# Kernel optimization log

Hardware: AMD Instinct MI355X
Metric: run time of the kernel (lower is better)

## Reference

```python
import jax, jax.numpy as jnp
import numpy as np

N_NODES = 50000
N_EDGES = 600000
F_IN = 128
HID = 128
N_GRAPHS = 512
N_CLASSES = 2


def _sage_conv(x, src, dst, Wl, Wr, b, n_nodes):
    # PyG SAGEConv (aggr='mean'): out = lin_l(mean_{j in N(i)} x_j) + lin_r(x_i)
    msg_sum = jax.ops.segment_sum(x[src], dst, num_segments=n_nodes)  # [N, F]
    deg = jax.ops.segment_sum(jnp.ones((src.shape[0],), x.dtype), dst, num_segments=n_nodes)
    agg = msg_sum / jnp.maximum(deg, 1.0)[:, None]
    return agg @ Wl + b + x @ Wr


def setup_inputs() -> dict:
    key = jax.random.key(0)
    ks = jax.random.split(key, 16)
    x = jax.random.normal(ks[0], (N_NODES, F_IN), dtype=jnp.float32)
    edge_index = jax.random.randint(ks[1], (2, N_EDGES), 0, N_NODES, dtype=jnp.int64)
    batch = jnp.sort(jax.random.randint(ks[2], (N_NODES,), 0, N_GRAPHS, dtype=jnp.int64))
    inp = {"x": x, "edge_index": edge_index, "batch": batch, "num_graphs": N_GRAPHS}
    # SAGEConv params (glorot-ish scale)
    dims = [(F_IN, HID), (HID, HID), (HID, HID), (HID, HID)]
    for i, (din, dout) in enumerate(dims, start=1):
        s = 1.0 / np.sqrt(din)
        inp[f"Wl{i}"] = jax.random.normal(ks[2 + 3 * i], (din, dout), dtype=jnp.float32) * s
        inp[f"Wr{i}"] = jax.random.normal(ks[3 + 3 * i], (din, dout), dtype=jnp.float32) * s
        inp[f"b{i}"] = jnp.zeros((dout,), dtype=jnp.float32)
    inp["Wf1"] = jax.random.normal(ks[3], (HID, 128), dtype=jnp.float32) / np.sqrt(HID)
    inp["bf1"] = jnp.zeros((128,), dtype=jnp.float32)
    inp["Wf2"] = jax.random.normal(ks[4], (128, N_CLASSES), dtype=jnp.float32) / np.sqrt(128.0)
    inp["bf2"] = jnp.zeros((N_CLASSES,), dtype=jnp.float32)
    return inp


def reference(x, edge_index, batch, num_graphs,
              Wl1, Wr1, b1, Wl2, Wr2, b2, Wl3, Wr3, b3, Wl4, Wr4, b4,
              Wf1, bf1, Wf2, bf2):
    src, dst = edge_index[0], edge_index[1]
    n = x.shape[0]
    h = jax.nn.relu(_sage_conv(x, src, dst, Wl1, Wr1, b1, n))
    h = jax.nn.relu(_sage_conv(h, src, dst, Wl2, Wr2, b2, n))
    h = jax.nn.relu(_sage_conv(h, src, dst, Wl3, Wr3, b3, n))
    h = jax.nn.relu(_sage_conv(h, src, dst, Wl4, Wr4, b4, n))
    # global_mean_pool over graphs
    pooled_sum = jax.ops.segment_sum(h, batch, num_segments=num_graphs)
    counts = jax.ops.segment_sum(jnp.ones((n,), h.dtype), batch, num_segments=num_graphs)
    pooled = pooled_sum / jnp.maximum(counts, 1.0)[:, None]
    emb = pooled @ Wf1 + bf1
    # dropout p=0.5 is identity in eval mode
    out = emb @ Wf2 + bf2
    return out
```

## Files before the change

### kernel.cpp

```cpp
#include <hip/hip_runtime.h>

#define N_NODES   50000
#define N_EDGES   600000
#define F         128
#define N_GRAPHS  512
#define MROWS     32
#define ASTRIDE   264
#define NB_SCAN   196
#define ECAP      1536

typedef short  short8 __attribute__((ext_vector_type(8)));
typedef short  short4_t __attribute__((ext_vector_type(4)));
typedef float  f32x4  __attribute__((ext_vector_type(4)));

__device__ __forceinline__ void split_bf16(float v, short& hi, short& lo) {
    unsigned u  = __float_as_uint(v);
    unsigned hb = u & 0xFFFF0000u;
    hi = (short)(u >> 16);
    float rem = v - __uint_as_float(hb);
    lo = (short)(__float_as_uint(rem) >> 16);
}

__device__ __forceinline__ void split4(float x, float y, float z, float w,
                                       short4_t& hi, short4_t& lo) {
    short h, l;
    split_bf16(x, h, l); hi[0] = h; lo[0] = l;
    split_bf16(y, h, l); hi[1] = h; lo[1] = l;
    split_bf16(z, h, l); hi[2] = h; lo[2] = l;
    split_bf16(w, h, l); hi[3] = h; lo[3] = l;
}

__global__ void deg_int_kernel(const int* __restrict__ dst, int* __restrict__ deg) {
    int e = blockIdx.x * blockDim.x + threadIdx.x;
    if (e < N_EDGES) atomicAdd(&deg[dst[e]], 1);
}

__global__ __launch_bounds__(256) void bsum_kernel(const int* __restrict__ deg,
                                                   int* __restrict__ bsum) {
    int i = blockIdx.x * 256 + threadIdx.x;
    int v = (i < N_NODES) ? deg[i] : 0;
    #pragma unroll
    for (int off = 32; off > 0; off >>= 1) v += __shfl_down(v, off, 64);
    __shared__ int wsum[4];
    int lane = threadIdx.x & 63, w = threadIdx.x >> 6;
    if (lane == 0) wsum[w] = v;
    __syncthreads();
    if (threadIdx.x == 0) bsum[blockIdx.x] = wsum[0] + wsum[1] + wsum[2] + wsum[3];
}

__global__ __launch_bounds__(256) void p2_kernel(
    int* __restrict__ bsum,
    const float* __restrict__ Wl0, const float* __restrict__ Wr0,
    const float* __restrict__ Wl1, const float* __restrict__ Wr1,
    const float* __restrict__ Wl2, const float* __restrict__ Wr2,
    const float* __restrict__ Wl3, const float* __restrict__ Wr3,
    short* __restrict__ wtbase)
{
    if (blockIdx.x == 0) {
        __shared__ int s[256];
        int t = threadIdx.x;
        int v = (t < NB_SCAN) ? bsum[t] : 0;
        s[t] = v;
        __syncthreads();
        for (int off = 1; off < 256; off <<= 1) {
            int x = s[t];
            int add = (t >= off) ? s[t - off] : 0;
            __syncthreads();
            s[t] = x + add;
            __syncthreads();
        }
        bsum[t] = (t == 0) ? 0 : s[t - 1];
    } else {
        int gt = (blockIdx.x - 1) * 256 + threadIdx.x;
        int l  = gt >> 15;
        int t  = gt & 32767;
        const float* Wl; const float* Wr;
        switch (l) {
            case 0:  Wl = Wl0; Wr = Wr0; break;
            case 1:  Wl = Wl1; Wr = Wr1; break;
            case 2:  Wl = Wl2; Wr = Wr2; break;
            default: Wl = Wl3; Wr = Wr3; break;
        }
        int n = t >> 8, k = t & 255;
        float w = (k < F) ? Wl[k * F + n] : Wr[(k - F) * F + n];
        short h, lo;
        split_bf16(w, h, lo);
        short* hi_plane = wtbase + (size_t)l * 65536;
        hi_plane[t]         = h;
        hi_plane[32768 + t] = lo;
    }
}

__global__ __launch_bounds__(256) void scan_apply_kernel(
    const int* __restrict__ deg, const int* __restrict__ boff,
    int* __restrict__ row_start, int* __restrict__ cursor,
    float* __restrict__ inv_deg)
{
    __shared__ int s[256];
    int b = blockIdx.x, t = threadIdx.x;
    int i = b * 256 + t;
    int d = (i < N_NODES) ? deg[i] : 0;
    s[t] = d;
    __syncthreads();
    for (int off = 1; off < 256; off <<= 1) {
        int x = s[t];
        int add = (t >= off) ? s[t - off] : 0;
        __syncthreads();
        s[t] = x + add;
        __syncthreads();
    }
    int excl = s[t] - d + boff[b];
    if (i < N_NODES) {
        row_start[i] = excl;
        cursor[i]    = excl;
        inv_deg[i]   = 1.0f / fmaxf((float)d, 1.0f);
    }
    if (b == 0 && t == 0) row_start[N_NODES] = N_EDGES;
}

__global__ void fill_kernel(const int* __restrict__ src, const int* __restrict__ dst,
                            int* __restrict__ cursor, int* __restrict__ eidx) {
    int e = blockIdx.x * blockDim.x + threadIdx.x;
    if (e < N_EDGES) {
        int p = atomicAdd(&cursor[dst[e]], 1);
        eidx[p] = src[e];
    }
}

__global__ __launch_bounds__(512) void layer_kernel(
    const float* __restrict__ h_in, const int* __restrict__ row_start,
    const int* __restrict__ eidx, const float* __restrict__ inv_deg,
    const short* __restrict__ wt_hi, const short* __restrict__ wt_lo,
    const float* __restrict__ b, float* __restrict__ h_out)
{
    __shared__ short Ahi[MROWS][ASTRIDE];
    __shared__ short Alo[MROWS][ASTRIDE];
    __shared__ int   eshare[ECAP];

    const int t    = threadIdx.x;
    const int base = blockIdx.x * MROWS;

    const int blk_end = (base + MROWS < N_NODES) ? base + MROWS : N_NODES;
    const int s_blk0  = row_start[base];
    const int s_blk1  = row_start[blk_end];
    const int ecnt    = s_blk1 - s_blk0;
    const bool use_lds = (ecnt <= ECAP);
    if (use_lds) {
        for (int i = t; i < ecnt; i += 512) eshare[i] = eidx[s_blk0 + i];
    }
    __syncthreads();

    {
        const int c4   = t & 31;
        const int rr   = t >> 5;
        const int rowA = base + rr;
        const int rowB = rowA + 16;
        const bool vB  = (rowB < N_NODES);

        int a0 = row_start[rowA] - s_blk0, a1 = row_start[rowA + 1] - s_blk0;
        int b0 = 0, b1 = 0;
        if (vB) { b0 = row_start[rowB] - s_blk0; b1 = row_start[rowB + 1] - s_blk0; }
        const int na = a1 - a0, nb = b1 - b0;

        float scA = inv_deg[rowA];
        float scB = vB ? inv_deg[rowB] : 0.0f;

        float4 sA = ((const float4*)(h_in + (size_t)rowA * F))[c4];
        float4 sB = {0, 0, 0, 0};
        if (vB) sB = ((const float4*)(h_in + (size_t)rowB * F))[c4];

        f32x4 aA = {0, 0, 0, 0}, aB = {0, 0, 0, 0};
        const int mx = na > nb ? na : nb;
        for (int eo = 0; eo < mx; eo += 4) {
            int   idxA[4], idxB[4];
            float mA[4], mB[4];
            #pragma unroll
            for (int u = 0; u < 4; ++u) {
                bool okA = (eo + u) < na;
                bool okB = (eo + u) < nb;
                int offA = okA ? a0 + eo + u : 0;
                int offB = okB ? b0 + eo + u : 0;
                int ia = use_lds ? eshare[offA] : eidx[s_blk0 + offA];
                int ib = use_lds ? eshare[offB] : eidx[s_blk0 + offB];
                idxA[u] = okA ? ia : 0;
                idxB[u] = okB ? ib : 0;
                mA[u] = okA ? 1.0f : 0.0f;
                mB[u] = okB ? 1.0f : 0.0f;
            }
            #pragma unroll
            for (int u = 0; u < 4; ++u) {
                float4 va = ((const float4*)(h_in + (size_t)idxA[u] * F))[c4];
                float4 vb = ((const float4*)(h_in + (size_t)idxB[u] * F))[c4];
                aA[0] = fmaf(va.x, mA[u], aA[0]);
                aA[1] = fmaf(va.y, mA[u], aA[1]);
                aA[2] = fmaf(va.z, mA[u], aA[2]);
                aA[3] = fmaf(va.w, mA[u], aA[3]);
                aB[0] = fmaf(vb.x, mB[u], aB[0]);
                aB[1] = fmaf(vb.y, mB[u], aB[1]);
                aB[2] = fmaf(vb.z, mB[u], aB[2]);
                aB[3] = fmaf(vb.w, mB[u], aB[3]);
            }
        }

        short4_t h4, l4;
        split4(aA[0] * scA, aA[1] * scA, aA[2] * scA, aA[3] * scA, h4, l4);
        *(short4_t*)&Ahi[rr][c4 * 4] = h4;
        *(short4_t*)&Alo[rr][c4 * 4] = l4;
        split4(sA.x, sA.y, sA.z, sA.w, h4, l4);
        *(short4_t*)&Ahi[rr][F + c4 * 4] = h4;
        *(short4_t*)&Alo[rr][F + c4 * 4] = l4;

        split4(aB[0] * scB, aB[1] * scB, aB[2] * scB, aB[3] * scB, h4, l4);
        *(short4_t*)&Ahi[rr + 16][c4 * 4] = h4;
        *(short4_t*)&Alo[rr + 16][c4 * 4] = l4;
        split4(sB.x, sB.y, sB.z, sB.w, h4, l4);
        *(short4_t*)&Ahi[rr + 16][F + c4 * 4] = h4;
        *(short4_t*)&Alo[rr + 16][F + c4 * 4] = l4;
    }
    __syncthreads();

    const int w    = t >> 6;
    const int lane = t & 63;
    const int m    = lane & 15;
    const int quad = lane >> 4;
    const int n0   = w * 16 + m;

    f32x4 acc0 = {0,0,0,0};
    f32x4 acc1 = {0,0,0,0};

    #pragma unroll
    for (int ks = 0; ks < 8; ++ks) {
        const int ko = ks * 32 + quad * 8;
        short8 ah0 = *(const short8*)&Ahi[m][ko];
        short8 ah1 = *(const short8*)&Ahi[16 + m][ko];
        short8 al0 = *(const short8*)&Alo[m][ko];
        short8 al1 = *(const short8*)&Alo[16 + m][ko];
        short8 bh  = *(const short8*)&wt_hi[(size_t)n0 * 256 + ko];
        short8 bl  = *(const short8*)&wt_lo[(size_t)n0 * 256 + ko];

        acc0 = __builtin_amdgcn_mfma_f32_16x16x32_bf16(ah0, bh, acc0, 0, 0, 0);
        acc0 = __builtin_amdgcn_mfma_f32_16x16x32_bf16(ah0, bl, acc0, 0, 0, 0);
        acc0 = __builtin_amdgcn_mfma_f32_16x16x32_bf16(al0, bh, acc0, 0, 0, 0);

        acc1 = __builtin_amdgcn_mfma_f32_16x16x32_bf16(ah1, bh, acc1, 0, 0, 0);
        acc1 = __builtin_amdgcn_mfma_f32_16x16x32_bf16(ah1, bl, acc1, 0, 0, 0);
        acc1 = __builtin_amdgcn_mfma_f32_16x16x32_bf16(al1, bh, acc1, 0, 0, 0);
    }

    float bj = b[n0];
    #pragma unroll
    for (int reg = 0; reg < 4; ++reg) {
        int r0 = base + quad * 4 + reg;
        int r1 = r0 + 16;
        if (r0 < N_NODES) h_out[(size_t)r0 * F + n0] = fmaxf(acc0[reg] + bj, 0.0f);
        if (r1 < N_NODES) h_out[(size_t)r1 * F + n0] = fmaxf(acc1[reg] + bj, 0.0f);
    }
}

__global__ __launch_bounds__(128) void poolhead_kernel(
    const int* __restrict__ batch, const float* __restrict__ h,
    const float* __restrict__ Wf1, const float* __restrict__ bf1,
    const float* __restrict__ Wf2, const float* __restrict__ bf2,
    float* __restrict__ out)
{
    int g = blockIdx.x;
    int j = threadIdx.x;
    int lo = 0, hi = N_NODES;
    while (lo < hi) { int m = (lo + hi) >> 1; if (batch[m] < g) lo = m + 1; else hi = m; }
    int start = lo;
    hi = N_NODES;
    while (lo < hi) { int m = (lo + hi) >> 1; if (batch[m] <= g) lo = m + 1; else hi = m; }
    int end = lo;

    float acc = 0.0f;
    int r = start;
    for (; r + 4 <= end; r += 4) {
        float v0 = h[(size_t)(r + 0) * F + j];
        float v1 = h[(size_t)(r + 1) * F + j];
        float v2 = h[(size_t)(r + 2) * F + j];
        float v3 = h[(size_t)(r + 3) * F + j];
        acc += (v0 + v1) + (v2 + v3);
    }
    for (; r < end; ++r) acc += h[(size_t)r * F + j];

    __shared__ float p[F];
    __shared__ float emb[F];
    p[j] = acc / fmaxf((float)(end - start), 1.0f);
    __syncthreads();
    float e = bf1[j];
    #pragma unroll 8
    for (int k = 0; k < F; ++k) e += p[k] * Wf1[k * F + j];
    emb[j] = e;
    __syncthreads();
    if (j < 2) {
        float o = bf2[j];
        for (int k = 0; k < F; ++k) o += emb[k] * Wf2[k * 2 + j];
        out[(size_t)g * 2 + j] = o;
    }
}

extern "C" void kernel_launch(void* const* d_in, const int* in_sizes, int n_in,
                              void* d_out, int out_size, void* d_ws, size_t ws_size,
                              hipStream_t stream) {
    const float* x     = (const float*)d_in[0];
    const int*   ei    = (const int*)d_in[1];
    const int*   src   = ei;
    const int*   dst   = ei + N_EDGES;
    const int*   batch = (const int*)d_in[2];
    const float* Wl[4] = {(const float*)d_in[4],  (const float*)d_in[7],
                          (const float*)d_in[10], (const float*)d_in[13]};
    const float* Wr[4] = {(const float*)d_in[5],  (const float*)d_in[8],
                          (const float*)d_in[11], (const float*)d_in[14]};
    const float* bb[4] = {(const float*)d_in[6],  (const float*)d_in[9],
                          (const float*)d_in[12], (const float*)d_in[15]};
    const float* Wf1 = (const float*)d_in[16];
    const float* bf1 = (const float*)d_in[17];
    const float* Wf2 = (const float*)d_in[18];
    const float* bf2 = (const float*)d_in[19];
    float* out = (float*)d_out;

    float* ws = (float*)d_ws;
    const size_t HSZ = (size_t)N_NODES * F;
    float* B0        = ws;
    float* B1        = B0 + HSZ;
    float* inv_deg   = B1 + HSZ;
    int*   row_start = (int*)(inv_deg + N_NODES);
    int*   cursor    = row_start + N_NODES + 1;
    int*   eidx      = cursor + N_NODES;
    int*   deg_i     = eidx + N_EDGES;
    int*   bsum      = deg_i + N_NODES;
    short* wtbase    = (short*)(bsum + 256);

    (void)hipMemsetAsync(deg_i, 0, N_NODES * sizeof(int), stream);

    deg_int_kernel<<<(N_EDGES + 255) / 256, 256, 0, stream>>>(dst, deg_i);
    bsum_kernel<<<NB_SCAN, 256, 0, stream>>>(deg_i, bsum);
    p2_kernel<<<513, 256, 0, stream>>>(bsum,
        Wl[0], Wr[0], Wl[1], Wr[1], Wl[2], Wr[2], Wl[3], Wr[3], wtbase);
    scan_apply_kernel<<<NB_SCAN, 256, 0, stream>>>(deg_i, bsum, row_start, cursor, inv_deg);
    fill_kernel<<<(N_EDGES + 255) / 256, 256, 0, stream>>>(src, dst, cursor, eidx);

    const int layer_blocks = (N_NODES + MROWS - 1) / MROWS;
    const float* hin = x;
    float* buf[2] = {B0, B1};
    for (int l = 0; l < 4; ++l) {
        float* tgt = buf[l & 1];
        const short* whi = wtbase + (size_t)l * 65536;
        const short* wlo = whi + 32768;
        layer_kernel<<<layer_blocks, 512, 0, stream>>>(
            hin, row_start, eidx, inv_deg, whi, wlo, bb[l], tgt);
        hin = tgt;
    }

    poolhead_kernel<<<N_GRAPHS, 128, 0, stream>>>(batch, hin, Wf1, bf1, Wf2, bf2, out);
}
```

Before: 469.8 us.

## Store node features in bf16 to halve gather traffic across layers

Converts the input features to bf16 in a new pre-pass, and stores every layer's output activations as bf16 instead of fp32. The neighbour gather and the pooling read packed bf16 and widen to fp32 for accumulation, so each gathered row moves half the bytes. The self term is no longer split into hi/lo parts, since it is already exact bf16. The gather is also restructured to one row per 16 threads with 8-wide edge unrolling, and the LDS staging of edge indices is dropped. The cost is lower precision in the activations and the risk of exceeding the accuracy tolerance.

```diff
diff --git a/kernel.cpp b/kernel.cpp
--- a/kernel.cpp
+++ b/kernel.cpp
@@ -7,11 +7,11 @@
 #define MROWS     32
 #define ASTRIDE   264
 #define NB_SCAN   196
-#define ECAP      1536
-
-typedef short  short8 __attribute__((ext_vector_type(8)));
-typedef short  short4_t __attribute__((ext_vector_type(4)));
-typedef float  f32x4  __attribute__((ext_vector_type(4)));
+
+typedef short          short8   __attribute__((ext_vector_type(8)));
+typedef short          short4_t __attribute__((ext_vector_type(4)));
+typedef float          f32x4    __attribute__((ext_vector_type(4)));
+typedef unsigned int   uint4_t  __attribute__((ext_vector_type(4)));
 
 __device__ __forceinline__ void split_bf16(float v, short& hi, short& lo) {
     unsigned u  = __float_as_uint(v);
@@ -21,18 +21,29 @@
     lo = (short)(__float_as_uint(rem) >> 16);
 }
 
-__device__ __forceinline__ void split4(float x, float y, float z, float w,
-                                       short4_t& hi, short4_t& lo) {
-    short h, l;
-    split_bf16(x, h, l); hi[0] = h; lo[0] = l;
-    split_bf16(y, h, l); hi[1] = h; lo[1] = l;
-    split_bf16(z, h, l); hi[2] = h; lo[2] = l;
-    split_bf16(w, h, l); hi[3] = h; lo[3] = l;
+__device__ __forceinline__ unsigned short f2bf_rne(float f) {
+    unsigned u = __float_as_uint(f);
+    u += 0x7FFFu + ((u >> 16) & 1u);
+    return (unsigned short)(u >> 16);
 }
 
 __global__ void deg_int_kernel(const int* __restrict__ dst, int* __restrict__ deg) {
     int e = blockIdx.x * blockDim.x + threadIdx.x;
     if (e < N_EDGES) atomicAdd(&deg[dst[e]], 1);
+}
+
+__global__ __launch_bounds__(256) void x2bf_kernel(const float* __restrict__ x,
+                                                   unsigned short* __restrict__ xb) {
+    int i = blockIdx.x * 256 + threadIdx.x;
+    if (i >= (N_NODES * F) / 8) return;
+    float4 a = ((const float4*)x)[2 * i];
+    float4 b = ((const float4*)x)[2 * i + 1];
+    short8 o;
+    o[0] = (short)f2bf_rne(a.x); o[1] = (short)f2bf_rne(a.y);
+    o[2] = (short)f2bf_rne(a.z); o[3] = (short)f2bf_rne(a.w);
+    o[4] = (short)f2bf_rne(b.x); o[5] = (short)f2bf_rne(b.y);
+    o[6] = (short)f2bf_rne(b.z); o[7] = (short)f2bf_rne(b.w);
+    ((short8*)xb)[i] = o;
 }
 
 __global__ __launch_bounds__(256) void bsum_kernel(const int* __restrict__ deg,
@@ -128,94 +139,74 @@
 }
 
 __global__ __launch_bounds__(512) void layer_kernel(
-    const float* __restrict__ h_in, const int* __restrict__ row_start,
+    const unsigned short* __restrict__ hb_in, const int* __restrict__ row_start,
     const int* __restrict__ eidx, const float* __restrict__ inv_deg,
     const short* __restrict__ wt_hi, const short* __restrict__ wt_lo,
-    const float* __restrict__ b, float* __restrict__ h_out)
+    const float* __restrict__ b, unsigned short* __restrict__ hb_out)
 {
     __shared__ short Ahi[MROWS][ASTRIDE];
     __shared__ short Alo[MROWS][ASTRIDE];
-    __shared__ int   eshare[ECAP];
 
     const int t    = threadIdx.x;
     const int base = blockIdx.x * MROWS;
 
-    const int blk_end = (base + MROWS < N_NODES) ? base + MROWS : N_NODES;
-    const int s_blk0  = row_start[base];
-    const int s_blk1  = row_start[blk_end];
-    const int ecnt    = s_blk1 - s_blk0;
-    const bool use_lds = (ecnt <= ECAP);
-    if (use_lds) {
-        for (int i = t; i < ecnt; i += 512) eshare[i] = eidx[s_blk0 + i];
-    }
-    __syncthreads();
-
     {
-        const int c4   = t & 31;
-        const int rr   = t >> 5;
-        const int rowA = base + rr;
-        const int rowB = rowA + 16;
-        const bool vB  = (rowB < N_NODES);
-
-        int a0 = row_start[rowA] - s_blk0, a1 = row_start[rowA + 1] - s_blk0;
-        int b0 = 0, b1 = 0;
-        if (vB) { b0 = row_start[rowB] - s_blk0; b1 = row_start[rowB + 1] - s_blk0; }
-        const int na = a1 - a0, nb = b1 - b0;
-
-        float scA = inv_deg[rowA];
-        float scB = vB ? inv_deg[rowB] : 0.0f;
-
-        float4 sA = ((const float4*)(h_in + (size_t)rowA * F))[c4];
-        float4 sB = {0, 0, 0, 0};
-        if (vB) sB = ((const float4*)(h_in + (size_t)rowB * F))[c4];
-
-        f32x4 aA = {0, 0, 0, 0}, aB = {0, 0, 0, 0};
-        const int mx = na > nb ? na : nb;
-        for (int eo = 0; eo < mx; eo += 4) {
-            int   idxA[4], idxB[4];
-            float mA[4], mB[4];
+        const int c8  = t & 15;
+        const int rr  = t >> 4;
+        const int row = base + rr;
+        const bool v  = (row < N_NODES);
+
+        int a0 = 0, na = 0;
+        float sc = 0.0f;
+        if (v) {
+            a0 = row_start[row];
+            na = row_start[row + 1] - a0;
+            sc = inv_deg[row];
+        }
+
+        short8 selfv = {0,0,0,0,0,0,0,0};
+        if (v) selfv = *(const short8*)(hb_in + (size_t)row * F + c8 * 8);
+
+        float acc[8] = {0,0,0,0,0,0,0,0};
+        for (int eo = 0; eo < na; eo += 8) {
+            int   idx[8];
+            float msk[8];
             #pragma unroll
-            for (int u = 0; u < 4; ++u) {
-                bool okA = (eo + u) < na;
-                bool okB = (eo + u) < nb;
-                int offA = okA ? a0 + eo + u : 0;
-                int offB = okB ? b0 + eo + u : 0;
-                int ia = use_lds ? eshare[offA] : eidx[s_blk0 + offA];
-                int ib = use_lds ? eshare[offB] : eidx[s_blk0 + offB];
-                idxA[u] = okA ? ia : 0;
-                idxB[u] = okB ? ib : 0;
-                mA[u] = okA ? 1.0f : 0.0f;
-                mB[u] = okB ? 1.0f : 0.0f;
+            for (int u = 0; u < 8; ++u) {
+                bool ok = (eo + u) < na;
+                int  sl = ok ? a0 + eo + u : a0;
+                int  ia = eidx[sl];
+                idx[u] = ok ? ia : 0;
+                msk[u] = ok ? 1.0f : 0.0f;
             }
             #pragma unroll
-            for (int u = 0; u < 4; ++u) {
-                float4 va = ((const float4*)(h_in + (size_t)idxA[u] * F))[c4];
-                float4 vb = ((const float4*)(h_in + (size_t)idxB[u] * F))[c4];
-                aA[0] = fmaf(va.x, mA[u], aA[0]);
-                aA[1] = fmaf(va.y, mA[u], aA[1]);
-                aA[2] = fmaf(va.z, mA[u], aA[2]);
-                aA[3] = fmaf(va.w, mA[u], aA[3]);
-                aB[0] = fmaf(vb.x, mB[u], aB[0]);
-                aB[1] = fmaf(vb.y, mB[u], aB[1]);
-                aB[2] = fmaf(vb.z, mB[u], aB[2]);
-                aB[3] = fmaf(vb.w, mB[u], aB[3]);
+            for (int u = 0; u < 8; ++u) {
+                short8 hv = *(const short8*)(hb_in + (size_t)idx[u] * F + c8 * 8);
+                uint4_t uw = *(const uint4_t*)&hv;
+                #pragma unroll
+                for (int q = 0; q < 4; ++q) {
+                    unsigned wq = uw[q];
+                    float flo = __uint_as_float(wq << 16);
+                    float fhi = __uint_as_float(wq & 0xFFFF0000u);
+                    acc[2 * q]     = fmaf(flo, msk[u], acc[2 * q]);
+                    acc[2 * q + 1] = fmaf(fhi, msk[u], acc[2 * q + 1]);
+                }
             }
         }
 
-        short4_t h4, l4;
-        split4(aA[0] * scA, aA[1] * scA, aA[2] * scA, aA[3] * scA, h4, l4);
-        *(short4_t*)&Ahi[rr][c4 * 4] = h4;
-        *(short4_t*)&Alo[rr][c4 * 4] = l4;
-        split4(sA.x, sA.y, sA.z, sA.w, h4, l4);
-        *(short4_t*)&Ahi[rr][F + c4 * 4] = h4;
-        *(short4_t*)&Alo[rr][F + c4 * 4] = l4;
-
-        split4(aB[0] * scB, aB[1] * scB, aB[2] * scB, aB[3] * scB, h4, l4);
-        *(short4_t*)&Ahi[rr + 16][c4 * 4] = h4;
-        *(short4_t*)&Alo[rr + 16][c4 * 4] = l4;
-        split4(sB.x, sB.y, sB.z, sB.w, h4, l4);
-        *(short4_t*)&Ahi[rr + 16][F + c4 * 4] = h4;
-        *(short4_t*)&Alo[rr + 16][F + c4 * 4] = l4;
+        short8 h8, l8;
+        #pragma unroll
+        for (int k = 0; k < 8; ++k) {
+            short h, l;
+            split_bf16(acc[k] * sc, h, l);
+            h8[k] = h; l8[k] = l;
+        }
+        *(short8*)&Ahi[rr][c8 * 8] = h8;
+        *(short8*)&Alo[rr][c8 * 8] = l8;
+
+        short8 z8 = {0,0,0,0,0,0,0,0};
+        *(short8*)&Ahi[rr][F + c8 * 8] = selfv;
+        *(short8*)&Alo[rr][F + c8 * 8] = z8;
     }
     __syncthreads();
 
@@ -252,13 +243,15 @@
     for (int reg = 0; reg < 4; ++reg) {
         int r0 = base + quad * 4 + reg;
         int r1 = r0 + 16;
-        if (r0 < N_NODES) h_out[(size_t)r0 * F + n0] = fmaxf(acc0[reg] + bj, 0.0f);
-        if (r1 < N_NODES) h_out[(size_t)r1 * F + n0] = fmaxf(acc1[reg] + bj, 0.0f);
+        if (r0 < N_NODES)
+            hb_out[(size_t)r0 * F + n0] = f2bf_rne(fmaxf(acc0[reg] + bj, 0.0f));
+        if (r1 < N_NODES)
+            hb_out[(size_t)r1 * F + n0] = f2bf_rne(fmaxf(acc1[reg] + bj, 0.0f));
     }
 }
 
 __global__ __launch_bounds__(128) void poolhead_kernel(
-    const int* __restrict__ batch, const float* __restrict__ h,
+    const int* __restrict__ batch, const unsigned short* __restrict__ hb,
     const float* __restrict__ Wf1, const float* __restrict__ bf1,
     const float* __restrict__ Wf2, const float* __restrict__ bf2,
     float* __restrict__ out)
@@ -275,13 +268,14 @@
     float acc = 0.0f;
     int r = start;
     for (; r + 4 <= end; r += 4) {
-        float v0 = h[(size_t)(r + 0) * F + j];
-        float v1 = h[(size_t)(r + 1) * F + j];
-        float v2 = h[(size_t)(r + 2) * F + j];
-        float v3 = h[(size_t)(r + 3) * F + j];
+        float v0 = __uint_as_float((unsigned)hb[(size_t)(r + 0) * F + j] << 16);
+        float v1 = __uint_as_float((unsigned)hb[(size_t)(r + 1) * F + j] << 16);
+        float v2 = __uint_as_float((unsigned)hb[(size_t)(r + 2) * F + j] << 16);
+        float v3 = __uint_as_float((unsigned)hb[(size_t)(r + 3) * F + j] << 16);
         acc += (v0 + v1) + (v2 + v3);
     }
-    for (; r < end; ++r) acc += h[(size_t)r * F + j];
+    for (; r < end; ++r)
+        acc += __uint_as_float((unsigned)hb[(size_t)r * F + j] << 16);
 
     __shared__ float p[F];
     __shared__ float emb[F];
@@ -319,11 +313,11 @@
     const float* bf2 = (const float*)d_in[19];
     float* out = (float*)d_out;
 
-    float* ws = (float*)d_ws;
     const size_t HSZ = (size_t)N_NODES * F;
-    float* B0        = ws;
-    float* B1        = B0 + HSZ;
-    float* inv_deg   = B1 + HSZ;
+    unsigned short* XB  = (unsigned short*)d_ws;
+    unsigned short* HB0 = XB + HSZ;
+    unsigned short* HB1 = HB0 + HSZ;
+    float* inv_deg   = (float*)(HB1 + HSZ);
     int*   row_start = (int*)(inv_deg + N_NODES);
     int*   cursor    = row_start + N_NODES + 1;
     int*   eidx      = cursor + N_NODES;
@@ -339,12 +333,13 @@
         Wl[0], Wr[0], Wl[1], Wr[1], Wl[2], Wr[2], Wl[3], Wr[3], wtbase);
     scan_apply_kernel<<<NB_SCAN, 256, 0, stream>>>(deg_i, bsum, row_start, cursor, inv_deg);
     fill_kernel<<<(N_EDGES + 255) / 256, 256, 0, stream>>>(src, dst, cursor, eidx);
+    x2bf_kernel<<<(int)((HSZ / 8 + 255) / 256), 256, 0, stream>>>(x, XB);
 
     const int layer_blocks = (N_NODES + MROWS - 1) / MROWS;
-    const float* hin = x;
-    float* buf[2] = {B0, B1};
+    const unsigned short* hin = XB;
+    unsigned short* buf[2] = {HB0, HB1};
     for (int l = 0; l < 4; ++l) {
-        float* tgt = buf[l & 1];
+        unsigned short* tgt = buf[l & 1];
         const short* whi = wtbase + (size_t)l * 65536;
         const short* wlo = whi + 32768;
         layer_kernel<<<layer_blocks, 512, 0, stream>>>(
```

Measured after the change: 409.1 us. 12.9% less time.
